# Performance work log

Hardware: AMD Instinct MI355X
Metric: run time of the kernel (lower is better)

## Reference

```python
import jax, jax.numpy as jnp
import numpy as np

N_NODES = 50000
N_EDGES = 800000
NUM_FEATS = 512
NUM_CLASSES = 64
NUM_LAYERS = 4


def setup_inputs() -> dict:
    key = jax.random.key(0)
    k1, k2, k3 = jax.random.split(key, 3)
    x = jax.random.normal(k1, (N_NODES, NUM_FEATS), dtype=jnp.float32)
    # glorot init for weight [num_feats, num_classes]
    scale = jnp.sqrt(6.0 / (NUM_FEATS + NUM_CLASSES)).astype(jnp.float32)
    weight = jax.random.uniform(k2, (NUM_FEATS, NUM_CLASSES), dtype=jnp.float32,
                                minval=-scale, maxval=scale)
    edge_index = jax.random.randint(k3, (2, N_EDGES), 0, N_NODES, dtype=jnp.int64)
    return {"x": x, "weight": weight, "edge_index": edge_index}


def reference(x, weight, edge_index):
    row, col = edge_index[0], edge_index[1]  # [E], [E]
    # symmetric GCN normalization: deg^{-1/2}[row] * deg^{-1/2}[col]
    deg = jax.ops.segment_sum(jnp.ones((edge_index.shape[1],), dtype=x.dtype),
                              row, num_segments=x.shape[0])  # [N]
    deg_inv_sqrt = jnp.where(deg > 0, jax.lax.rsqrt(jnp.maximum(deg, 1e-12)), 0.0)
    norm = (deg_inv_sqrt[row] * deg_inv_sqrt[col])[:, None]  # [E, 1]

    h = x @ weight  # [N, num_classes] (dropout skipped: eval mode)
    for _ in range(NUM_LAYERS):
        # gather source features, scale by edge norm, scatter-add to destinations
        msg = norm * h[row]  # [E, num_classes]
        h = jax.ops.segment_sum(msg, col, num_segments=x.shape[0])  # [N, num_classes]
        # type_norm == 'None' -> layers_bn is identity
    return h
```

## Files before the change

### kernel.cpp

```cpp
#include <hip/hip_runtime.h>
#include <hip/hip_fp16.h>

#define NFEAT 512
#define NCLS  64
#define NNODES 50000
#define NW    (NNODES / 4)
#define NB    256
#define SLOTS 64

typedef unsigned int uint;
using short8 = __attribute__((ext_vector_type(8))) short;
using f32x4  = __attribute__((ext_vector_type(4))) float;

static __device__ __forceinline__ unsigned short f32_to_bf16_rne(float f) {
    unsigned u = __float_as_uint(f);
    unsigned r = u + 0x7FFFu + ((u >> 16) & 1u);
    return (unsigned short)(r >> 16);
}
static __device__ __forceinline__ float bf16_to_f32(unsigned short b) {
    return __uint_as_float(((unsigned)b) << 16);
}
static __device__ __forceinline__ uint cvt_pk_bf16(float a, float b) {
    uint r;
    asm("v_cvt_pk_bf16_f32 %0, %1, %2" : "=v"(r) : "v"(a), "v"(b));
    return r;
}
static __device__ __forceinline__ void split_bf16x8(const float* xs, short8& ahi, short8& alo) {
    union { uint u[4]; short8 s; } H, L;
#pragma unroll
    for (int t = 0; t < 4; ++t) {
        float x0 = xs[2 * t], x1 = xs[2 * t + 1];
        uint hp = cvt_pk_bf16(x0, x1);
        float f0 = __uint_as_float(hp << 16);
        float f1 = __uint_as_float(hp & 0xffff0000u);
        uint lp = cvt_pk_bf16(x0 - f0, x1 - f1);
        H.u[t] = hp; L.u[t] = lp;
    }
    ahi = H.s; alo = L.s;
}


__global__ __launch_bounds__(256) void hist_packw_kernel(
        const int* __restrict__ row, const int* __restrict__ col,
        const float* __restrict__ w,
        uint* __restrict__ degB, uint* __restrict__ cntB,
        short8* __restrict__ wp, int E, int CH) {
    __shared__ __align__(16) uint h[2 * NW];
    int b = blockIdx.x;
    if (b < NB) {
        for (int i = threadIdx.x; i < 2 * NW; i += 256) h[i] = 0;
        __syncthreads();
        int e0 = b * CH, e1 = min(E, e0 + CH);
        for (int e = e0 + threadIdx.x; e < e1; e += 256) {
            int c = col[e], r = row[e];
            atomicAdd(&h[c >> 2], 1u << ((c & 3) * 8));
            atomicAdd(&h[NW + (r >> 2)], 1u << ((r & 3) * 8));
        }
        __syncthreads();
        uint4* cb = reinterpret_cast<uint4*>(cntB + (size_t)b * NW);
        uint4* db = reinterpret_cast<uint4*>(degB + (size_t)b * NW);
        const uint4* c4 = reinterpret_cast<const uint4*>(h);
        const uint4* d4 = reinterpret_cast<const uint4*>(h + NW);
        for (int i = threadIdx.x; i < NW / 4; i += 256) cb[i] = c4[i];
        for (int i = threadIdx.x; i < NW / 4; i += 256) db[i] = d4[i];
        return;
    }
    int gid = (b - NB) * 256 + threadIdx.x;
    int lane = gid & 63;
    int F = gid >> 6;
    int s = F & 1;
    int nt = (F >> 1) & 3;
    int kk = F >> 3;
    int k0 = kk * 32 + (lane >> 4) * 8;
    int c  = nt * 16 + (lane & 15);
    short8 v;
#pragma unroll
    for (int j = 0; j < 8; ++j) {
        float xv = w[(k0 + j) * NCLS + c];
        unsigned short hi = f32_to_bf16_rne(xv);
        unsigned short outv = hi;
        if (s) outv = f32_to_bf16_rne(xv - bf16_to_f32(hi));
        v[j] = (short)outv;
    }
    wp[gid] = v;
}


__global__ __launch_bounds__(256) void reduce_kernel(uint* __restrict__ cntB,
                                                     const uint* __restrict__ degB,
                                                     int* __restrict__ cntTot,
                                                     float* __restrict__ dinv) {
    int gid = blockIdx.x * 256 + threadIdx.x;
    if (gid < NW) {
        int wi = gid;
        uint run = 0;
#pragma unroll 8
        for (int b = 0; b < NB; ++b) {
            uint v = cntB[(size_t)b * NW + wi];
            cntB[(size_t)b * NW + wi] = run;
            run += v;
        }
        int4 t = { (int)(run & 255), (int)((run >> 8) & 255),
                   (int)((run >> 16) & 255), (int)(run >> 24) };
        *reinterpret_cast<int4*>(cntTot + wi * 4) = t;
    } else if (gid < 2 * NW) {
        int wi = gid - NW;
        uint run = 0;
#pragma unroll 8
        for (int b = 0; b < NB; ++b) run += degB[(size_t)b * NW + wi];
        int d0 = run & 255, d1 = (run >> 8) & 255, d2 = (run >> 16) & 255, d3 = run >> 24;
        float4 dv;
        dv.x = d0 ? rsqrtf((float)d0) : 0.0f;
        dv.y = d1 ? rsqrtf((float)d1) : 0.0f;
        dv.z = d2 ? rsqrtf((float)d2) : 0.0f;
        dv.w = d3 ? rsqrtf((float)d3) : 0.0f;
        *reinterpret_cast<float4*>(dinv + wi * 4) = dv;
    }
}


__global__ __launch_bounds__(256) void place_kernel(
        const int* __restrict__ row, const int* __restrict__ col,
        const uint* __restrict__ offB, int* __restrict__ slots,
        int E, int CH) {
    __shared__ __align__(16) uint sh[NW];
    int b = blockIdx.x;
    uint4* c4 = reinterpret_cast<uint4*>(sh);
    const uint4* o4 = reinterpret_cast<const uint4*>(offB + (size_t)b * NW);
    for (int i = threadIdx.x; i < NW / 4; i += 256) c4[i] = o4[i];
    __syncthreads();
    int e0 = b * CH, e1 = min(E, e0 + CH);
    for (int e = e0 + threadIdx.x; e < e1; e += 256) {
        int c = col[e];
        uint old = atomicAdd(&sh[c >> 2], 1u << ((c & 3) * 8));
        int pos = (old >> ((c & 3) * 8)) & 255;
        if (pos < SLOTS) slots[(c << 6) + pos] = row[e];
    }
}


__global__ __launch_bounds__(256, 4) void matmul_sort_kernel(
        const float* __restrict__ x, const short8* __restrict__ wp,
        const float* __restrict__ dinv, __half* __restrict__ u0,
        int* __restrict__ slots, const int* __restrict__ cntTot,
        int N, int nmm) {
    int b = blockIdx.x;
    int tid = threadIdx.x;
    int wave = tid >> 6, lane = tid & 63;

    if (b >= nmm) {
        int base = (b - nmm) * 16 + wave * 4;
#pragma unroll
        for (int k = 0; k < 4; ++k) {
            int wid = base + k;
            if (wid >= N) break;
            int cq = cntTot[wid];
            cq = (cq < SLOTS) ? cq : SLOTS;
            int* sl = slots + (wid << 6);
            int v = (lane < cq) ? sl[lane] : 0x7fffffff;
#pragma unroll
            for (int kk = 2; kk <= 64; kk <<= 1) {
#pragma unroll
                for (int j = kk >> 1; j >= 1; j >>= 1) {
                    int p = __shfl_xor(v, j);
                    int lo = min(v, p), hi = max(v, p);
                    bool up = ((lane & kk) == 0);
                    v = (((lane & j) == 0) == up) ? lo : hi;
                }
            }
            if (lane < cq) sl[lane] = v;
        }
        return;
    }

    int rlo = lane & 15, khi = lane >> 4;
    int row0 = b * 64 + wave * 16;
    int rn = row0 + rlo; if (rn > N - 1) rn = N - 1;
    const float* xr = x + (size_t)rn * NFEAT + khi * 8;

    f32x4 acc[4];
#pragma unroll
    for (int nt = 0; nt < 4; ++nt) acc[nt] = f32x4{0.f, 0.f, 0.f, 0.f};

    const short8* fbase = wp + lane;
    float4 xa = *reinterpret_cast<const float4*>(xr);
    float4 xb = *reinterpret_cast<const float4*>(xr + 4);

#pragma unroll
    for (int it = 0; it < 16; ++it) {
        const short8* fb = fbase + it * 512;
        short8 bf0 = fb[0],   bf1 = fb[64];
        short8 bf2 = fb[128], bf3 = fb[192];
        short8 bf4 = fb[256], bf5 = fb[320];
        short8 bf6 = fb[384], bf7 = fb[448];

        float4 nxa, nxb;
        if (it < 15) {
            nxa = *reinterpret_cast<const float4*>(xr + (it + 1) * 32);
            nxb = *reinterpret_cast<const float4*>(xr + (it + 1) * 32 + 4);
        }

        float xs[8] = {xa.x, xa.y, xa.z, xa.w, xb.x, xb.y, xb.z, xb.w};
        short8 ahi, alo;
        split_bf16x8(xs, ahi, alo);
        acc[0] = __builtin_amdgcn_mfma_f32_16x16x32_bf16(ahi, bf0, acc[0], 0, 0, 0);
        acc[1] = __builtin_amdgcn_mfma_f32_16x16x32_bf16(ahi, bf2, acc[1], 0, 0, 0);
        acc[2] = __builtin_amdgcn_mfma_f32_16x16x32_bf16(ahi, bf4, acc[2], 0, 0, 0);
        acc[3] = __builtin_amdgcn_mfma_f32_16x16x32_bf16(ahi, bf6, acc[3], 0, 0, 0);
        acc[0] = __builtin_amdgcn_mfma_f32_16x16x32_bf16(alo, bf0, acc[0], 0, 0, 0);
        acc[1] = __builtin_amdgcn_mfma_f32_16x16x32_bf16(alo, bf2, acc[1], 0, 0, 0);
        acc[2] = __builtin_amdgcn_mfma_f32_16x16x32_bf16(alo, bf4, acc[2], 0, 0, 0);
        acc[3] = __builtin_amdgcn_mfma_f32_16x16x32_bf16(alo, bf6, acc[3], 0, 0, 0);
        acc[0] = __builtin_amdgcn_mfma_f32_16x16x32_bf16(ahi, bf1, acc[0], 0, 0, 0);
        acc[1] = __builtin_amdgcn_mfma_f32_16x16x32_bf16(ahi, bf3, acc[1], 0, 0, 0);
        acc[2] = __builtin_amdgcn_mfma_f32_16x16x32_bf16(ahi, bf5, acc[2], 0, 0, 0);
        acc[3] = __builtin_amdgcn_mfma_f32_16x16x32_bf16(ahi, bf7, acc[3], 0, 0, 0);

        if (it < 15) { xa = nxa; xb = nxb; }
    }

    int rbase = row0 + khi * 4;
#pragma unroll
    for (int j = 0; j < 4; ++j) {
        int r = rbase + j;
        if (r < N) {
            float dn = dinv[r];
            __half* op = u0 + ((size_t)r << 6) + rlo;
            op[0]  = __float2half(acc[0][j] * dn);
            op[16] = __float2half(acc[1][j] * dn);
            op[32] = __float2half(acc[2][j] * dn);
            op[48] = __float2half(acc[3][j] * dn);
        }
    }
}


__global__ __launch_bounds__(256) void gather_kernel(const __half* __restrict__ u,
                                                     const int* __restrict__ cntTot,
                                                     const int* __restrict__ slots,
                                                     const float* __restrict__ dinv,
                                                     __half* __restrict__ out_h,
                                                     float* __restrict__ out_f,
                                                     int N, int sq) {
    int wid = blockIdx.x * 4 + (threadIdx.x >> 6);
    if (wid >= N) return;
    int lane = threadIdx.x & 63;
    int q = lane >> 3;
    int p = lane & 7;
    int cq = cntTot[wid];
    cq = (cq < SLOTS) ? cq : SLOTS;
    const int* sl = slots + (wid << 6);
    int s_l = sl[lane];

    float a0=0.f,a1=0.f,a2=0.f,a3=0.f,a4=0.f,a5=0.f,a6=0.f,a7=0.f;
    float b0=0.f,b1=0.f,b2=0.f,b3=0.f,b4=0.f,b5=0.f,b6=0.f,b7=0.f;
#pragma unroll
    for (int j = 0; j < 8; j += 2) {
        int i0 = q + 8 * j;
        int i1 = q + 8 * (j + 1);
        int s0 = __shfl(s_l, i0);
        int s1 = __shfl(s_l, i1);
        if (i0 < cq) {
            uint4 d0 = *reinterpret_cast<const uint4*>(u + ((size_t)s0 << 6) + p * 8);
            float2 f0 = __half22float2(*reinterpret_cast<__half2*>(&d0.x));
            float2 f1 = __half22float2(*reinterpret_cast<__half2*>(&d0.y));
            float2 f2 = __half22float2(*reinterpret_cast<__half2*>(&d0.z));
            float2 f3 = __half22float2(*reinterpret_cast<__half2*>(&d0.w));
            a0 += f0.x; a1 += f0.y; a2 += f1.x; a3 += f1.y;
            a4 += f2.x; a5 += f2.y; a6 += f3.x; a7 += f3.y;
        }
        if (i1 < cq) {
            uint4 d1 = *reinterpret_cast<const uint4*>(u + ((size_t)s1 << 6) + p * 8);
            float2 g0 = __half22float2(*reinterpret_cast<__half2*>(&d1.x));
            float2 g1 = __half22float2(*reinterpret_cast<__half2*>(&d1.y));
            float2 g2 = __half22float2(*reinterpret_cast<__half2*>(&d1.z));
            float2 g3 = __half22float2(*reinterpret_cast<__half2*>(&d1.w));
            b0 += g0.x; b1 += g0.y; b2 += g1.x; b3 += g1.y;
            b4 += g2.x; b5 += g2.y; b6 += g3.x; b7 += g3.y;
        }
    }
    a0 += b0; a1 += b1; a2 += b2; a3 += b3;
    a4 += b4; a5 += b5; a6 += b6; a7 += b7;
#pragma unroll
    for (int off = 8; off < 64; off <<= 1) {
        a0 += __shfl_xor(a0, off); a1 += __shfl_xor(a1, off);
        a2 += __shfl_xor(a2, off); a3 += __shfl_xor(a3, off);
        a4 += __shfl_xor(a4, off); a5 += __shfl_xor(a5, off);
        a6 += __shfl_xor(a6, off); a7 += __shfl_xor(a7, off);
    }
    if (q == 0) {
        float sc = dinv[wid];
        if (sq) {
            sc *= sc;
            __half2 h0 = __floats2half2_rn(a0 * sc, a1 * sc);
            __half2 h1 = __floats2half2_rn(a2 * sc, a3 * sc);
            __half2 h2 = __floats2half2_rn(a4 * sc, a5 * sc);
            __half2 h3 = __floats2half2_rn(a6 * sc, a7 * sc);
            uint4 d;
            d.x = *reinterpret_cast<uint*>(&h0);
            d.y = *reinterpret_cast<uint*>(&h1);
            d.z = *reinterpret_cast<uint*>(&h2);
            d.w = *reinterpret_cast<uint*>(&h3);
            *reinterpret_cast<uint4*>(out_h + ((size_t)wid << 6) + p * 8) = d;
        } else {
            float4 r0 = {a0 * sc, a1 * sc, a2 * sc, a3 * sc};
            float4 r1 = {a4 * sc, a5 * sc, a6 * sc, a7 * sc};
            float4* op = reinterpret_cast<float4*>(out_f + ((size_t)wid << 6) + p * 8);
            op[0] = r0;
            op[1] = r1;
        }
    }
}


extern "C" void kernel_launch(void* const* d_in, const int* in_sizes, int n_in,
                              void* d_out, int out_size, void* d_ws, size_t ws_size,
                              hipStream_t stream) {
    const float* x = (const float*)d_in[0];
    const float* w = (const float*)d_in[1];
    const int*   ei = (const int*)d_in[2];

    int N = in_sizes[0] / NFEAT;
    int E = in_sizes[2] / 2;
    const int* row = ei;
    const int* col = ei + E;
    float* out = (float*)d_out;

    auto align256 = [](size_t v) { return (v + 255) & ~(size_t)255; };
    char* ws = (char*)d_ws;
    size_t off = 0;
    uint* cntB   = (uint*)(ws + off);   off += align256((size_t)NB * NW * sizeof(uint));
    uint* degB   = (uint*)(ws + off);   off += align256((size_t)NB * NW * sizeof(uint));
    int* cntTot  = (int*)(ws + off);    off += align256((size_t)NNODES * sizeof(int));
    float* dinv  = (float*)(ws + off);  off += align256((size_t)NNODES * sizeof(float));
    short8* wp   = (short8*)(ws + off); off += align256((size_t)8192 * sizeof(short8));
    int* slots   = (int*)(ws + off);    off += align256((size_t)NNODES * SLOTS * sizeof(int));
    __half* uA   = (__half*)(ws + off); off += align256((size_t)NNODES * NCLS * sizeof(__half));
    __half* uB   = (__half*)(ws + off); off += align256((size_t)NNODES * NCLS * sizeof(__half));

    int CH = (E + NB - 1) / NB;

    hist_packw_kernel<<<NB + 32, 256, 0, stream>>>(row, col, w, degB, cntB, wp, E, CH);
    reduce_kernel<<<(2 * NW + 255) / 256, 256, 0, stream>>>(cntB, degB, cntTot, dinv);
    place_kernel<<<NB, 256, 0, stream>>>(row, col, cntB, slots, E, CH);
    int nmm = (N + 63) / 64;
    int nsort = (N + 15) / 16;
    matmul_sort_kernel<<<nmm + nsort, 256, 0, stream>>>(x, wp, dinv, uA,
                                                        slots, cntTot, N, nmm);

    int ngrid = (N + 3) / 4;
    gather_kernel<<<ngrid, 256, 0, stream>>>(uA, cntTot, slots, dinv, uB, nullptr, N, 1);
    gather_kernel<<<ngrid, 256, 0, stream>>>(uB, cntTot, slots, dinv, uA, nullptr, N, 1);
    gather_kernel<<<ngrid, 256, 0, stream>>>(uA, cntTot, slots, dinv, uB, nullptr, N, 1);
    gather_kernel<<<ngrid, 256, 0, stream>>>(uB, cntTot, slots, dinv, nullptr, out, N, 0);
}
```

Measured before the change: 174.6 us.

## Stage packed weights in LDS with persistent matmul grid and split out sort kernel

After: 180.5 us. +3.4%, slower.

```diff
diff --git a/kernel.cpp b/kernel.cpp
--- a/kernel.cpp
+++ b/kernel.cpp
@@ -139,99 +139,102 @@
 }
 
 
-__global__ __launch_bounds__(256, 4) void matmul_sort_kernel(
+__global__ __launch_bounds__(512, 1) void matmul_kernel(
         const float* __restrict__ x, const short8* __restrict__ wp,
-        const float* __restrict__ dinv, __half* __restrict__ u0,
-        int* __restrict__ slots, const int* __restrict__ cntTot,
-        int N, int nmm) {
-    int b = blockIdx.x;
+        const float* __restrict__ dinv, __half* __restrict__ u0, int N) {
+    __shared__ short8 blds[8192];
     int tid = threadIdx.x;
+    for (int i = tid; i < 8192; i += 512) blds[i] = wp[i];
+    __syncthreads();
+
     int wave = tid >> 6, lane = tid & 63;
-
-    if (b >= nmm) {
-        int base = (b - nmm) * 16 + wave * 4;
-#pragma unroll
-        for (int k = 0; k < 4; ++k) {
-            int wid = base + k;
-            if (wid >= N) break;
-            int cq = cntTot[wid];
-            cq = (cq < SLOTS) ? cq : SLOTS;
-            int* sl = slots + (wid << 6);
-            int v = (lane < cq) ? sl[lane] : 0x7fffffff;
-#pragma unroll
-            for (int kk = 2; kk <= 64; kk <<= 1) {
-#pragma unroll
-                for (int j = kk >> 1; j >= 1; j >>= 1) {
-                    int p = __shfl_xor(v, j);
-                    int lo = min(v, p), hi = max(v, p);
-                    bool up = ((lane & kk) == 0);
-                    v = (((lane & j) == 0) == up) ? lo : hi;
-                }
+    int rlo = lane & 15, khi = lane >> 4;
+    int ngroups = (N + 15) >> 4;
+    int stride = gridDim.x * 8;
+
+    for (int g = blockIdx.x * 8 + wave; g < ngroups; g += stride) {
+        int row0 = g << 4;
+        int rn = row0 + rlo; if (rn > N - 1) rn = N - 1;
+        const float* xr = x + (size_t)rn * NFEAT + khi * 8;
+
+        f32x4 acc[4];
+#pragma unroll
+        for (int nt = 0; nt < 4; ++nt) acc[nt] = f32x4{0.f, 0.f, 0.f, 0.f};
+
+        float4 xa = *reinterpret_cast<const float4*>(xr);
+        float4 xb = *reinterpret_cast<const float4*>(xr + 4);
+
+#pragma unroll
+        for (int it = 0; it < 16; ++it) {
+            const short8* fb = blds + it * 512 + lane;
+            short8 bf0 = fb[0],   bf1 = fb[64];
+            short8 bf2 = fb[128], bf3 = fb[192];
+            short8 bf4 = fb[256], bf5 = fb[320];
+            short8 bf6 = fb[384], bf7 = fb[448];
+
+            float4 nxa, nxb;
+            if (it < 15) {
+                nxa = *reinterpret_cast<const float4*>(xr + (it + 1) * 32);
+                nxb = *reinterpret_cast<const float4*>(xr + (it + 1) * 32 + 4);
             }
-            if (lane < cq) sl[lane] = v;
-        }
-        return;
-    }
-
-    int rlo = lane & 15, khi = lane >> 4;
-    int row0 = b * 64 + wave * 16;
-    int rn = row0 + rlo; if (rn > N - 1) rn = N - 1;
-    const float* xr = x + (size_t)rn * NFEAT + khi * 8;
-
-    f32x4 acc[4];
-#pragma unroll
-    for (int nt = 0; nt < 4; ++nt) acc[nt] = f32x4{0.f, 0.f, 0.f, 0.f};
-
-    const short8* fbase = wp + lane;
-    float4 xa = *reinterpret_cast<const float4*>(xr);
-    float4 xb = *reinterpret_cast<const float4*>(xr + 4);
-
-#pragma unroll
-    for (int it = 0; it < 16; ++it) {
-        const short8* fb = fbase + it * 512;
-        short8 bf0 = fb[0],   bf1 = fb[64];
-        short8 bf2 = fb[128], bf3 = fb[192];
-        short8 bf4 = fb[256], bf5 = fb[320];
-        short8 bf6 = fb[384], bf7 = fb[448];
-
-        float4 nxa, nxb;
-        if (it < 15) {
-            nxa = *reinterpret_cast<const float4*>(xr + (it + 1) * 32);
-            nxb = *reinterpret_cast<const float4*>(xr + (it + 1) * 32 + 4);
-        }
-
-        float xs[8] = {xa.x, xa.y, xa.z, xa.w, xb.x, xb.y, xb.z, xb.w};
-        short8 ahi, alo;
-        split_bf16x8(xs, ahi, alo);
-        acc[0] = __builtin_amdgcn_mfma_f32_16x16x32_bf16(ahi, bf0, acc[0], 0, 0, 0);
-        acc[1] = __builtin_amdgcn_mfma_f32_16x16x32_bf16(ahi, bf2, acc[1], 0, 0, 0);
-        acc[2] = __builtin_amdgcn_mfma_f32_16x16x32_bf16(ahi, bf4, acc[2], 0, 0, 0);
-        acc[3] = __builtin_amdgcn_mfma_f32_16x16x32_bf16(ahi, bf6, acc[3], 0, 0, 0);
-        acc[0] = __builtin_amdgcn_mfma_f32_16x16x32_bf16(alo, bf0, acc[0], 0, 0, 0);
-        acc[1] = __builtin_amdgcn_mfma_f32_16x16x32_bf16(alo, bf2, acc[1], 0, 0, 0);
-        acc[2] = __builtin_amdgcn_mfma_f32_16x16x32_bf16(alo, bf4, acc[2], 0, 0, 0);
-        acc[3] = __builtin_amdgcn_mfma_f32_16x16x32_bf16(alo, bf6, acc[3], 0, 0, 0);
-        acc[0] = __builtin_amdgcn_mfma_f32_16x16x32_bf16(ahi, bf1, acc[0], 0, 0, 0);
-        acc[1] = __builtin_amdgcn_mfma_f32_16x16x32_bf16(ahi, bf3, acc[1], 0, 0, 0);
-        acc[2] = __builtin_amdgcn_mfma_f32_16x16x32_bf16(ahi, bf5, acc[2], 0, 0, 0);
-        acc[3] = __builtin_amdgcn_mfma_f32_16x16x32_bf16(ahi, bf7, acc[3], 0, 0, 0);
-
-        if (it < 15) { xa = nxa; xb = nxb; }
-    }
-
-    int rbase = row0 + khi * 4;
-#pragma unroll
-    for (int j = 0; j < 4; ++j) {
-        int r = rbase + j;
-        if (r < N) {
-            float dn = dinv[r];
-            __half* op = u0 + ((size_t)r << 6) + rlo;
-            op[0]  = __float2half(acc[0][j] * dn);
-            op[16] = __float2half(acc[1][j] * dn);
-            op[32] = __float2half(acc[2][j] * dn);
-            op[48] = __float2half(acc[3][j] * dn);
-        }
-    }
+
+            float xs[8] = {xa.x, xa.y, xa.z, xa.w, xb.x, xb.y, xb.z, xb.w};
+            short8 ahi, alo;
+            split_bf16x8(xs, ahi, alo);
+            acc[0] = __builtin_amdgcn_mfma_f32_16x16x32_bf16(ahi, bf0, acc[0], 0, 0, 0);
+            acc[1] = __builtin_amdgcn_mfma_f32_16x16x32_bf16(ahi, bf2, acc[1], 0, 0, 0);
+            acc[2] = __builtin_amdgcn_mfma_f32_16x16x32_bf16(ahi, bf4, acc[2], 0, 0, 0);
+            acc[3] = __builtin_amdgcn_mfma_f32_16x16x32_bf16(ahi, bf6, acc[3], 0, 0, 0);
+            acc[0] = __builtin_amdgcn_mfma_f32_16x16x32_bf16(alo, bf0, acc[0], 0, 0, 0);
+            acc[1] = __builtin_amdgcn_mfma_f32_16x16x32_bf16(alo, bf2, acc[1], 0, 0, 0);
+            acc[2] = __builtin_amdgcn_mfma_f32_16x16x32_bf16(alo, bf4, acc[2], 0, 0, 0);
+            acc[3] = __builtin_amdgcn_mfma_f32_16x16x32_bf16(alo, bf6, acc[3], 0, 0, 0);
+            acc[0] = __builtin_amdgcn_mfma_f32_16x16x32_bf16(ahi, bf1, acc[0], 0, 0, 0);
+            acc[1] = __builtin_amdgcn_mfma_f32_16x16x32_bf16(ahi, bf3, acc[1], 0, 0, 0);
+            acc[2] = __builtin_amdgcn_mfma_f32_16x16x32_bf16(ahi, bf5, acc[2], 0, 0, 0);
+            acc[3] = __builtin_amdgcn_mfma_f32_16x16x32_bf16(ahi, bf7, acc[3], 0, 0, 0);
+
+            if (it < 15) { xa = nxa; xb = nxb; }
+        }
+
+        int rbase = row0 + khi * 4;
+#pragma unroll
+        for (int j = 0; j < 4; ++j) {
+            int r = rbase + j;
+            if (r < N) {
+                float dn = dinv[r];
+                __half* op = u0 + ((size_t)r << 6) + rlo;
+                op[0]  = __float2half(acc[0][j] * dn);
+                op[16] = __float2half(acc[1][j] * dn);
+                op[32] = __float2half(acc[2][j] * dn);
+                op[48] = __float2half(acc[3][j] * dn);
+            }
+        }
+    }
+}
+
+
+__global__ __launch_bounds__(256) void sort_kernel(int* __restrict__ slots,
+                                                   const int* __restrict__ cntTot,
+                                                   int N) {
+    int wid = blockIdx.x * 4 + (threadIdx.x >> 6);
+    if (wid >= N) return;
+    int lane = threadIdx.x & 63;
+    int cq = cntTot[wid];
+    cq = (cq < SLOTS) ? cq : SLOTS;
+    int* sl = slots + (wid << 6);
+    int v = (lane < cq) ? sl[lane] : 0x7fffffff;
+#pragma unroll
+    for (int k = 2; k <= 64; k <<= 1) {
+#pragma unroll
+        for (int j = k >> 1; j >= 1; j >>= 1) {
+            int p = __shfl_xor(v, j);
+            int lo = min(v, p), hi = max(v, p);
+            bool up = ((lane & k) == 0);
+            v = (((lane & j) == 0) == up) ? lo : hi;
+        }
+    }
+    if (lane < cq) sl[lane] = v;
 }
 
 
@@ -343,12 +346,10 @@
     hist_packw_kernel<<<NB + 32, 256, 0, stream>>>(row, col, w, degB, cntB, wp, E, CH);
     reduce_kernel<<<(2 * NW + 255) / 256, 256, 0, stream>>>(cntB, degB, cntTot, dinv);
     place_kernel<<<NB, 256, 0, stream>>>(row, col, cntB, slots, E, CH);
-    int nmm = (N + 63) / 64;
-    int nsort = (N + 15) / 16;
-    matmul_sort_kernel<<<nmm + nsort, 256, 0, stream>>>(x, wp, dinv, uA,
-                                                        slots, cntTot, N, nmm);
-
+    matmul_kernel<<<256, 512, 0, stream>>>(x, wp, dinv, uA, N);
     int ngrid = (N + 3) / 4;
+    sort_kernel<<<ngrid, 256, 0, stream>>>(slots, cntTot, N);
+
     gather_kernel<<<ngrid, 256, 0, stream>>>(uA, cntTot, slots, dinv, uB, nullptr, N, 1);
     gather_kernel<<<ngrid, 256, 0, stream>>>(uB, cntTot, slots, dinv, uA, nullptr, N, 1);
     gather_kernel<<<ngrid, 256, 0, stream>>>(uA, cntTot, slots, dinv, uB, nullptr, N, 1);
```
